# Kernel tuning notes

Hardware: AMD Instinct MI355X
Metric: run time of the kernel (lower is better)

Reference implementation:

```python
import jax, jax.numpy as jnp
import numpy as np

B, E, F = 16384, 128, 6
ITEM_V, CATE_V, HIST = 91718, 11, 50
I_IDX, J_IDX = np.triu_indices(F, k=1)  # 15 field pairs, loop order (0,1),(0,2),...
EPS = 1e-5


def _xavier(key, shape):
    fan_in, fan_out = shape[0], shape[-1]
    std = (2.0 / (fan_in + fan_out)) ** 0.5
    return std * jax.random.normal(key, shape, dtype=jnp.float32)


def setup_inputs() -> dict:
    key = jax.random.key(0)
    ks = jax.random.split(key, 20)
    inp = {
        'item_id': jax.random.randint(ks[0], (B,), 0, ITEM_V),
        'item_emb_d128': jax.random.normal(ks[1], (B, 128), dtype=jnp.float32),
        'likes_level': jax.random.randint(ks[2], (B,), 0, CATE_V),
        'views_level': jax.random.randint(ks[3], (B,), 0, CATE_V),
        'item_seq': jax.random.randint(ks[4], (B, HIST), 0, ITEM_V),
        # learned parameters
        'item_emb': 0.05 * jax.random.normal(ks[5], (ITEM_V, E), dtype=jnp.float32),
        'cate_emb': 0.05 * jax.random.normal(ks[6], (CATE_V, E), dtype=jnp.float32),
        'mm_W': _xavier(ks[7], (128, E)), 'mm_b': jnp.zeros((E,), jnp.float32),
        'ln_g': jnp.ones((E,), jnp.float32), 'ln_b': jnp.zeros((E,), jnp.float32),
        'se_W1': _xavier(ks[8], (F, F // 2)), 'se_b1': jnp.zeros((F // 2,), jnp.float32),
        'se_W2': _xavier(ks[9], (F // 2, F)), 'se_b2': jnp.zeros((F,), jnp.float32),
        'bi_W': _xavier(ks[10], (E, E)),
        'mlp_W1': _xavier(ks[11], (21 * E, 512)), 'mlp_b1': jnp.zeros((512,), jnp.float32),
        'bn1_g': jnp.ones((512,), jnp.float32), 'bn1_b': jnp.zeros((512,), jnp.float32),
        'bn1_rm': jnp.zeros((512,), jnp.float32), 'bn1_rv': jnp.ones((512,), jnp.float32),
        'mlp_W2': _xavier(ks[12], (512, 256)), 'mlp_b2': jnp.zeros((256,), jnp.float32),
        'bn2_g': jnp.ones((256,), jnp.float32), 'bn2_b': jnp.zeros((256,), jnp.float32),
        'bn2_rm': jnp.zeros((256,), jnp.float32), 'bn2_rv': jnp.ones((256,), jnp.float32),
        'mlp_W3': _xavier(ks[13], (256, 1)), 'mlp_b3': jnp.zeros((1,), jnp.float32),
    }
    return inp


def _forward(item_id, item_emb_d128, likes_level, views_level, item_seq,
             item_emb, cate_emb, mm_W, mm_b, ln_g, ln_b,
             se_W1, se_b1, se_W2, se_b2, bi_W,
             mlp_W1, mlp_b1, bn1_g, bn1_b, bn1_rm, bn1_rv,
             mlp_W2, mlp_b2, bn2_g, bn2_b, bn2_rm, bn2_rv,
             mlp_W3, mlp_b3):
    b = item_id.shape[0]
    tab = item_emb.at[0].set(0.0)  # padding_idx=0
    like_feat = cate_emb[likes_level]
    view_feat = cate_emb[views_level]
    item_feat = tab[item_id]
    # mm_proj: Linear -> LayerNorm -> ReLU
    mm = item_emb_d128 @ mm_W + mm_b
    mu = mm.mean(-1, keepdims=True)
    var = jnp.var(mm, axis=-1, keepdims=True)
    mm = jax.nn.relu((mm - mu) / jnp.sqrt(var + EPS) * ln_g + ln_b)
    # masked mean pooling over history
    seq_emb = tab[item_seq]                               # (B, HIST, E)
    valid = (item_seq != 0).astype(seq_emb.dtype)
    seq_sum = (seq_emb * valid[..., None]).sum(1)
    cnt = jnp.clip(valid.sum(1, keepdims=True), 1.0)
    hist_feat = seq_sum / cnt
    user_feat = jnp.zeros((b, E), seq_emb.dtype)
    x = jnp.stack([user_feat, like_feat, view_feat, item_feat, mm, hist_feat], axis=1)  # (B,6,E)
    # SENet
    z = x.mean(-1)
    w = jax.nn.sigmoid(jax.nn.relu(z @ se_W1 + se_b1) @ se_W2 + se_b2)
    xs = x * w[:, :, None]
    # bilinear 'all'
    xw = jnp.einsum('bfe,ed->bfd', xs, bi_W)
    p = xs[:, I_IDX, :] * xw[:, J_IDX, :]                 # (B,15,E)
    c = jnp.concatenate([xs.reshape(b, -1), p.reshape(b, -1)], axis=1)  # (B, 2688)
    # MLP head (eval mode: BN uses running stats, dropout off)
    h = c @ mlp_W1 + mlp_b1
    h = jax.nn.relu((h - bn1_rm) / jnp.sqrt(bn1_rv + EPS) * bn1_g + bn1_b)
    h = h @ mlp_W2 + mlp_b2
    h = jax.nn.relu((h - bn2_rm) / jnp.sqrt(bn2_rv + EPS) * bn2_g + bn2_b)
    logits = h @ mlp_W3 + mlp_b3
    return jax.nn.sigmoid(logits)[:, 0]


def reference(item_id, item_emb_d128, likes_level, views_level, item_seq,
              item_emb, cate_emb, mm_W, mm_b, ln_g, ln_b,
              se_W1, se_b1, se_W2, se_b2, bi_W,
              mlp_W1, mlp_b1, bn1_g, bn1_b, bn1_rm, bn1_rv,
              mlp_W2, mlp_b2, bn2_g, bn2_b, bn2_rm, bn2_rv,
              mlp_W3, mlp_b3):
    return _forward(item_id, item_emb_d128, likes_level, views_level, item_seq,
                    item_emb, cate_emb, mm_W, mm_b, ln_g, ln_b,
                    se_W1, se_b1, se_W2, se_b2, bi_W,
                    mlp_W1, mlp_b1, bn1_g, bn1_b, bn1_rm, bn1_rv,
                    mlp_W2, mlp_b2, bn2_g, bn2_b, bn2_rm, bn2_rv,
                    mlp_W3, mlp_b3)
```

## Files before the change

### kernel.cpp

```cpp
#include <hip/hip_runtime.h>
#include <hip/hip_bf16.h>

typedef __hip_bfloat16 bfloat;
typedef __bf16 bf16x8 __attribute__((ext_vector_type(8)));
typedef float f32x4 __attribute__((ext_vector_type(4)));

#define B_SZ   16384
#define E_DIM  128
#define HIST_L 50


#define IPACK 0x3221110000ULL
#define JPACK 0x3323213210ULL

__device__ __forceinline__ void gl_lds16(const void* g, void* l) {
    __builtin_amdgcn_global_load_lds(
        (const __attribute__((address_space(1))) unsigned int*)g,
        (__attribute__((address_space(3))) unsigned int*)l, 16, 0, 0);
}

__device__ __forceinline__ bf16x8 mul_bf16x8(bf16x8 a, bf16x8 b) {
    union { bf16x8 v; __hip_bfloat162 h[4]; } ua, ub, ur;
    ua.v = a; ub.v = b;
    #pragma unroll
    for (int i = 0; i < 4; ++i) ur.h[i] = __hmul2(ua.h[i], ub.h[i]);
    return ur.v;
}

__global__ __launch_bounds__(256) void feat_kernel(
    const int* __restrict__ item_id,
    const int* __restrict__ likes, const int* __restrict__ views,
    const int* __restrict__ seq,
    const float* __restrict__ item_emb, const float* __restrict__ cate_emb,
    const float* __restrict__ mm,
    const float* __restrict__ ln_g, const float* __restrict__ ln_b,
    const float* __restrict__ se_W1, const float* __restrict__ se_b1,
    const float* __restrict__ se_W2, const float* __restrict__ se_b2,
    bfloat* __restrict__ xs)
{
    const int tid = threadIdx.x;
    const int r   = tid >> 7;
    const int e   = tid & 127;
    const int b   = blockIdx.x * 2 + r;
    const int w   = tid >> 6;

    __shared__ float redh[2][4][128];
    __shared__ int   seq_s[2][64];
    __shared__ float lnred[4], lnred2[4];
    __shared__ float zred[5][4];
    __shared__ float wsh[2][6];
    __shared__ int   cnt_s[2];

    if (e < 64) seq_s[r][e] = (e < HIST_L) ? seq[(size_t)b * HIST_L + e] : 0;
    __syncthreads();

    const int iid = item_id[b];
    const float like_v = cate_emb[likes[b] * 128 + e];
    const float view_v = cate_emb[views[b] * 128 + e];
    const float item_raw = item_emb[(size_t)iid * 128 + e];
    const float item_v = iid ? item_raw : 0.f;
    const float acc = mm[(size_t)b * 128 + e];

    const int q   = e >> 5;
    const int l32 = e & 31;
    float4 hs = make_float4(0.f, 0.f, 0.f, 0.f);
    #pragma unroll
    for (int g = 0; g < 13; ++g) {
        int s = seq_s[r][g * 4 + q];
        const float4 v = *(const float4*)&item_emb[(size_t)s * 128 + l32 * 4];
        float m = (s != 0) ? 1.f : 0.f;
        hs.x = fmaf(v.x, m, hs.x);
        hs.y = fmaf(v.y, m, hs.y);
        hs.z = fmaf(v.z, m, hs.z);
        hs.w = fmaf(v.w, m, hs.w);
    }

    {
        float v = acc;
        #pragma unroll
        for (int off = 32; off > 0; off >>= 1) v += __shfl_down(v, off, 64);
        if ((tid & 63) == 0) lnred[w] = v;
    }
    __syncthreads();
    const float mu = (lnred[2 * r] + lnred[2 * r + 1]) * (1.f / 128.f);
    const float d  = acc - mu;
    {
        float v = d * d;
        #pragma unroll
        for (int off = 32; off > 0; off >>= 1) v += __shfl_down(v, off, 64);
        if ((tid & 63) == 0) lnred2[w] = v;
    }
    redh[r][q][l32 * 4 + 0] = hs.x;
    redh[r][q][l32 * 4 + 1] = hs.y;
    redh[r][q][l32 * 4 + 2] = hs.z;
    redh[r][q][l32 * 4 + 3] = hs.w;
    if ((w & 1) == 0 && e < 64) {
        bool valid = (e < HIST_L) && (seq_s[r][e] != 0);
        unsigned long long m = __ballot(valid);
        if (e == 0) cnt_s[r] = (int)__popcll(m);
    }
    __syncthreads();
    const float var = (lnred2[2 * r] + lnred2[2 * r + 1]) * (1.f / 128.f);
    float xmm = d * rsqrtf(var + 1e-5f) * ln_g[e] + ln_b[e];
    xmm = fmaxf(xmm, 0.f);

    const int cnt = cnt_s[r] > 0 ? cnt_s[r] : 1;
    const float hist_v = (redh[r][0][e] + redh[r][1][e] +
                          redh[r][2][e] + redh[r][3][e]) / (float)cnt;

    {
        float s1 = like_v, s2 = view_v, s3 = item_v, s4 = xmm, s5 = hist_v;
        #pragma unroll
        for (int off = 32; off > 0; off >>= 1) {
            s1 += __shfl_down(s1, off, 64);
            s2 += __shfl_down(s2, off, 64);
            s3 += __shfl_down(s3, off, 64);
            s4 += __shfl_down(s4, off, 64);
            s5 += __shfl_down(s5, off, 64);
        }
        if ((tid & 63) == 0) {
            zred[0][w] = s1; zred[1][w] = s2; zred[2][w] = s3;
            zred[3][w] = s4; zred[4][w] = s5;
        }
    }
    __syncthreads();

    if (e == 0) {
        float z[6];
        z[0] = 0.f;
        #pragma unroll
        for (int f = 1; f < 6; ++f)
            z[f] = (zred[f - 1][2 * r] + zred[f - 1][2 * r + 1]) * (1.f / 128.f);
        float a[3];
        #pragma unroll
        for (int j = 0; j < 3; ++j) {
            float s = se_b1[j];
            #pragma unroll
            for (int f = 0; f < 6; ++f) s += z[f] * se_W1[f * 3 + j];
            a[j] = fmaxf(s, 0.f);
        }
        #pragma unroll
        for (int f = 0; f < 6; ++f) {
            float s = se_b2[f];
            #pragma unroll
            for (int j = 0; j < 3; ++j) s += a[j] * se_W2[j * 6 + f];
            wsh[r][f] = 1.f / (1.f + expf(-s));
        }
    }
    __syncthreads();

    bfloat* xrow = xs + (size_t)b * 640;
    xrow[0 * 128 + e] = __float2bfloat16(like_v * wsh[r][1]);
    xrow[1 * 128 + e] = __float2bfloat16(view_v * wsh[r][2]);
    xrow[2 * 128 + e] = __float2bfloat16(item_v * wsh[r][3]);
    xrow[3 * 128 + e] = __float2bfloat16(xmm    * wsh[r][4]);
    xrow[4 * 128 + e] = __float2bfloat16(hist_v * wsh[r][5]);
}

__global__ __launch_bounds__(256) void transpose_f32_bf16(
    const float* __restrict__ in, bfloat* __restrict__ out, int K, int N)
{
    int idx = blockIdx.x * 256 + threadIdx.x;
    if (idx < K * N) {
        int k = idx / N, n = idx % N;
        out[(size_t)n * K + k] = __float2bfloat16(in[idx]);
    }
}

__global__ __launch_bounds__(256) void transpose_W1c(
    const float* __restrict__ W1, bfloat* __restrict__ W1t)
{
    int idx = blockIdx.x * 256 + threadIdx.x;
    if (idx < 512 * 1920) {
        int n = idx / 1920, kk = idx % 1920;
        int orig = kk + (kk < 640 ? 128 : 768);
        W1t[idx] = __float2bfloat16(W1[(size_t)orig * 512 + n]);
    }
}

__global__ __launch_bounds__(256) void bn_pre(
    const float* __restrict__ lb1, const float* __restrict__ g1,
    const float* __restrict__ bb1, const float* __restrict__ rm1,
    const float* __restrict__ rv1,
    const float* __restrict__ lb2, const float* __restrict__ g2,
    const float* __restrict__ bb2, const float* __restrict__ rm2,
    const float* __restrict__ rv2,
    const float* __restrict__ mm_b,
    float* __restrict__ S1, float* __restrict__ T1,
    float* __restrict__ S2, float* __restrict__ T2,
    float* __restrict__ Tmm)
{
    int j = blockIdx.x * 256 + threadIdx.x;
    if (j < 512) {
        float s = g1[j] * rsqrtf(rv1[j] + 1e-5f);
        S1[j] = s;
        T1[j] = (lb1[j] - rm1[j]) * s + bb1[j];
    } else if (j < 768) {
        int k = j - 512;
        float s = g2[k] * rsqrtf(rv2[k] + 1e-5f);
        S2[k] = s;
        T2[k] = (lb2[k] - rm2[k]) * s + bb2[k];
    } else if (j < 896) {
        Tmm[j - 768] = mm_b[j - 768];
    }
}

template<int MODE, int EPI, int MT, int NT, int F32OUT>
__global__ __launch_bounds__(256) void gemm_bt(
    const void* __restrict__ A, const bfloat* __restrict__ A2,
    const bfloat* __restrict__ Bt, void* __restrict__ C,
    int M, int N, int K,
    const float* __restrict__ S, const float* __restrict__ T)
{
    __shared__ __align__(16) short As[2][MT * 32];
    __shared__ __align__(16) short Bs[2][NT * 32];

    const int tid  = threadIdx.x;
    const int bm   = blockIdx.x * MT;
    const int bn   = blockIdx.y * NT;
    const int wave = tid >> 6;
    const int lane = tid & 63;
    const int wm   = (wave >> 1) * (MT / 2);
    const int wn   = (wave & 1) * (NT / 2);
    const int AF   = MT / 32;
    const int BF   = NT / 32;

    const short* Ag  = (const short*)A;
    const short* A2g = (const short*)A2;
    const short* Bg  = (const short*)Bt;

    f32x4 acc[MT / 32][NT / 32];
    #pragma unroll
    for (int i = 0; i < AF; ++i)
        #pragma unroll
        for (int j = 0; j < BF; ++j)
            acc[i][j] = (f32x4){0.f, 0.f, 0.f, 0.f};

    const int srow = tid >> 2;
    const int skc  = (tid & 3) * 8;

    for (int kt = 0; kt < K; kt += 64) {
        __syncthreads();
        #pragma unroll
        for (int h = 0; h < 2; ++h) {
            const int kk = kt + h * 32;
            #pragma unroll
            for (int r = 0; r < MT / 64; ++r) {
                int row = srow + r * 64;
                short* dst = &As[h][row * 32 + skc];
                if (MODE == 1) {
                    long rb = (long)(bm + row);
                    if (kk < 640) {
                        gl_lds16(&Ag[rb * 640 + kk + skc], dst);
                    } else {
                        int pp  = (kk - 640) >> 7;
                        int isl = (int)((IPACK >> (4 * pp)) & 15);
                        int jsl = (int)((JPACK >> (4 * pp)) & 15);
                        int e0  = ((kk - 640) & 127) + skc;
                        bf16x8 a = *(const bf16x8*)&Ag [rb * 640 + isl * 128 + e0];
                        bf16x8 b = *(const bf16x8*)&A2g[rb * 512 + jsl * 128 + e0];
                        *(bf16x8*)dst = mul_bf16x8(a, b);
                    }
                } else if (MODE == 2) {
                    int gr = bm + row;
                    gl_lds16(&Ag[((long)(gr >> 2)) * 640 +
                                 ((gr & 3) + 1) * 128 + kk + skc], dst);
                } else if (MODE == 3) {
                    const float* Af = (const float*)A;
                    long aoff = (long)(bm + row) * K + kk + skc;
                    float4 f0 = *(const float4*)&Af[aoff];
                    float4 f1 = *(const float4*)&Af[aoff + 4];
                    union { bf16x8 v; unsigned short s[8]; } u;
                    u.s[0] = __bfloat16_as_ushort(__float2bfloat16(f0.x));
                    u.s[1] = __bfloat16_as_ushort(__float2bfloat16(f0.y));
                    u.s[2] = __bfloat16_as_ushort(__float2bfloat16(f0.z));
                    u.s[3] = __bfloat16_as_ushort(__float2bfloat16(f0.w));
                    u.s[4] = __bfloat16_as_ushort(__float2bfloat16(f1.x));
                    u.s[5] = __bfloat16_as_ushort(__float2bfloat16(f1.y));
                    u.s[6] = __bfloat16_as_ushort(__float2bfloat16(f1.z));
                    u.s[7] = __bfloat16_as_ushort(__float2bfloat16(f1.w));
                    *(bf16x8*)dst = u.v;
                } else {
                    gl_lds16(&Ag[(long)(bm + row) * K + kk + skc], dst);
                }
            }
            #pragma unroll
            for (int r = 0; r < NT / 64; ++r) {
                int row = srow + r * 64;
                gl_lds16(&Bg[(long)(bn + row) * K + kk + skc],
                         &Bs[h][row * 32 + skc]);
            }
        }
        __syncthreads();

        const int koff  = (lane >> 4) * 8;
        const int rbase = lane & 15;
        #pragma unroll
        for (int h = 0; h < 2; ++h) {
            bf16x8 af[MT / 32], bfr[NT / 32];
            #pragma unroll
            for (int mt = 0; mt < AF; ++mt)
                af[mt] = *(const bf16x8*)
                    &As[h][(wm + mt * 16 + rbase) * 32 + koff];
            #pragma unroll
            for (int nt = 0; nt < BF; ++nt)
                bfr[nt] = *(const bf16x8*)
                    &Bs[h][(wn + nt * 16 + rbase) * 32 + koff];
            #pragma unroll
            for (int mt = 0; mt < AF; ++mt)
                #pragma unroll
                for (int nt = 0; nt < BF; ++nt)
                    acc[mt][nt] = __builtin_amdgcn_mfma_f32_16x16x32_bf16(
                        af[mt], bfr[nt], acc[mt][nt], 0, 0, 0);
        }
    }

    const int col0 = lane & 15;
    const int row0 = (lane >> 4) * 4;
    #pragma unroll
    for (int nt = 0; nt < BF; ++nt) {
        int col = bn + wn + nt * 16 + col0;
        float s = 1.f, t = 0.f;
        if (EPI) { s = (EPI == 1) ? S[col] : 1.f; t = T[col]; }
        #pragma unroll
        for (int mt = 0; mt < AF; ++mt) {
            #pragma unroll
            for (int i = 0; i < 4; ++i) {
                int row = bm + wm + mt * 16 + row0 + i;
                float v = acc[mt][nt][i];
                if (EPI == 1) v = fmaxf(v * s + t, 0.f);
                if (EPI == 2) v = v + t;
                if (F32OUT) ((float*)C)[(size_t)row * N + col] = v;
                else ((bfloat*)C)[(size_t)row * N + col] = __float2bfloat16(v);
            }
        }
    }
}

__global__ __launch_bounds__(256) void head_kernel(
    const bfloat* __restrict__ h2, const float* __restrict__ W3,
    const float* __restrict__ b3, float* __restrict__ out)
{
    int lane = threadIdx.x & 63;
    int row  = blockIdx.x * 4 + (threadIdx.x >> 6);
    float acc = 0.f;
    #pragma unroll
    for (int i = 0; i < 4; ++i)
        acc += __bfloat162float(h2[(size_t)row * 256 + i * 64 + lane]) *
               W3[i * 64 + lane];
    #pragma unroll
    for (int off = 32; off > 0; off >>= 1) acc += __shfl_down(acc, off, 64);
    if (lane == 0) {
        float l = acc + b3[0];
        out[row] = 1.f / (1.f + expf(-l));
    }
}

extern "C" void kernel_launch(void* const* d_in, const int* in_sizes, int n_in,
                              void* d_out, int out_size, void* d_ws, size_t ws_size,
                              hipStream_t stream) {
    const int*   item_id = (const int*)  d_in[0];
    const float* d128    = (const float*)d_in[1];
    const int*   likes   = (const int*)  d_in[2];
    const int*   views   = (const int*)  d_in[3];
    const int*   seq     = (const int*)  d_in[4];
    const float* item_emb= (const float*)d_in[5];
    const float* cate_emb= (const float*)d_in[6];
    const float* mm_W    = (const float*)d_in[7];
    const float* mm_b    = (const float*)d_in[8];
    const float* ln_g    = (const float*)d_in[9];
    const float* ln_b    = (const float*)d_in[10];
    const float* se_W1   = (const float*)d_in[11];
    const float* se_b1   = (const float*)d_in[12];
    const float* se_W2   = (const float*)d_in[13];
    const float* se_b2   = (const float*)d_in[14];
    const float* bi_W    = (const float*)d_in[15];
    const float* W1      = (const float*)d_in[16];
    const float* b1      = (const float*)d_in[17];
    const float* bn1_g   = (const float*)d_in[18];
    const float* bn1_b   = (const float*)d_in[19];
    const float* bn1_rm  = (const float*)d_in[20];
    const float* bn1_rv  = (const float*)d_in[21];
    const float* W2      = (const float*)d_in[22];
    const float* b2      = (const float*)d_in[23];
    const float* bn2_g   = (const float*)d_in[24];
    const float* bn2_b   = (const float*)d_in[25];
    const float* bn2_rm  = (const float*)d_in[26];
    const float* bn2_rv  = (const float*)d_in[27];
    const float* W3      = (const float*)d_in[28];
    const float* b3      = (const float*)d_in[29];

    const size_t fixed = 2300416;
    int CH = 1024;
    if      (fixed + (size_t)16384 * 3328 <= ws_size) CH = 16384;
    else if (fixed + (size_t)8192  * 3328 <= ws_size) CH = 8192;
    else if (fixed + (size_t)4096  * 3328 <= ws_size) CH = 4096;
    else if (fixed + (size_t)2048  * 3328 <= ws_size) CH = 2048;

    char* ws = (char*)d_ws;
    bfloat* W1t = (bfloat*)(ws);
    bfloat* W2t = (bfloat*)(ws + 1966080);
    bfloat* bWt = (bfloat*)(ws + 2228224);
    bfloat* mmWt= (bfloat*)(ws + 2260992);
    float*  S1  = (float*) (ws + 2293760);
    float*  T1  = (float*) (ws + 2295808);
    float*  S2  = (float*) (ws + 2297856);
    float*  T2  = (float*) (ws + 2298880);
    float*  Tmm = (float*) (ws + 2299904);
    bfloat* xs  = (bfloat*)(ws + fixed);
    bfloat* xw  = (bfloat*)(ws + fixed + (size_t)CH * 1280);
    bfloat* h1  = (bfloat*)(ws + fixed + (size_t)CH * 2304);
    bfloat* h2  = xw;
    float*  mm  = (float*)h1;

    transpose_W1c<<<(512 * 1920 + 255) / 256, 256, 0, stream>>>(W1, W1t);
    transpose_f32_bf16<<<(512 * 256 + 255) / 256, 256, 0, stream>>>(W2, W2t, 512, 256);
    transpose_f32_bf16<<<(128 * 128 + 255) / 256, 256, 0, stream>>>(bi_W, bWt, 128, 128);
    transpose_f32_bf16<<<(128 * 128 + 255) / 256, 256, 0, stream>>>(mm_W, mmWt, 128, 128);
    bn_pre<<<4, 256, 0, stream>>>(b1, bn1_g, bn1_b, bn1_rm, bn1_rv,
                                  b2, bn2_g, bn2_b, bn2_rm, bn2_rv,
                                  mm_b, S1, T1, S2, T2, Tmm);

    for (int off = 0; off < B_SZ; off += CH) {
        dim3 gmm(CH / 128, 128 / 64);
        gemm_bt<3, 2, 128, 64, 1><<<gmm, 256, 0, stream>>>(
            d128 + (size_t)off * 128, nullptr, mmWt, mm,
            CH, 128, 128, nullptr, Tmm);

        feat_kernel<<<CH / 2, 256, 0, stream>>>(
            item_id + off, likes + off, views + off,
            seq + (size_t)off * HIST_L, item_emb, cate_emb, mm,
            ln_g, ln_b, se_W1, se_b1, se_W2, se_b2, xs);

        dim3 gxw(CH * 4 / 128, 128 / 64);
        gemm_bt<2, 0, 128, 64, 0><<<gxw, 256, 0, stream>>>(
            xs, nullptr, bWt, xw, CH * 4, 128, 128, nullptr, nullptr);

        dim3 g1(CH / 128, 512 / 64);
        gemm_bt<1, 1, 128, 64, 0><<<g1, 256, 0, stream>>>(
            xs, xw, W1t, h1, CH, 512, 1920, S1, T1);

        dim3 g2(CH / 128, 256 / 64);
        gemm_bt<0, 1, 128, 64, 0><<<g2, 256, 0, stream>>>(
            h1, nullptr, W2t, h2, CH, 256, 512, S2, T2);

        head_kernel<<<CH / 4, 256, 0, stream>>>(h2, W3, b3, (float*)d_out + off);
    }
}
```

Measured before the change: 314.7 us.

## Double-buffer GEMM tiles with XOR-swizzled LDS layout

Restructures the bf16 MFMA GEMM so the next 64-wide K tile is staged into a second LDS buffer while the current one is consumed, with one barrier per iteration in place of two. The LDS tile layout becomes 64-column rows with an XOR swizzle on 16-byte chunks, applied both when staging from global memory and when reading fragments, to cut bank conflicts. The goal is to hide global load latency and reduce LDS conflicts. In exchange it doubles shared memory per block, which may lower occupancy, and adds index arithmetic.

After: 315.2 us. Within noise of the previous version (+0.2%).

```diff
diff --git a/kernel.cpp b/kernel.cpp
--- a/kernel.cpp
+++ b/kernel.cpp
@@ -212,8 +212,8 @@
     int M, int N, int K,
     const float* __restrict__ S, const float* __restrict__ T)
 {
-    __shared__ __align__(16) short As[2][MT * 32];
-    __shared__ __align__(16) short Bs[2][NT * 32];
+    __shared__ __align__(16) short As[2][MT * 64];
+    __shared__ __align__(16) short Bs[2][NT * 64];
 
     const int tid  = threadIdx.x;
     const int bm   = blockIdx.x * MT;
@@ -222,96 +222,122 @@
     const int lane = tid & 63;
     const int wm   = (wave >> 1) * (MT / 2);
     const int wn   = (wave & 1) * (NT / 2);
-    const int AF   = MT / 32;
-    const int BF   = NT / 32;
+    constexpr int AF = MT / 32;
+    constexpr int BF = NT / 32;
 
     const short* Ag  = (const short*)A;
     const short* A2g = (const short*)A2;
     const short* Bg  = (const short*)Bt;
 
-    f32x4 acc[MT / 32][NT / 32];
+    f32x4 acc[AF][BF];
     #pragma unroll
     for (int i = 0; i < AF; ++i)
         #pragma unroll
         for (int j = 0; j < BF; ++j)
             acc[i][j] = (f32x4){0.f, 0.f, 0.f, 0.f};
 
-    const int srow = tid >> 2;
-    const int skc  = (tid & 3) * 8;
-
-    for (int kt = 0; kt < K; kt += 64) {
-        __syncthreads();
+    const int srow = tid >> 3;
+    const int sck  = tid & 7;
+
+    auto stage = [&](int buf, int kt) {
+        #pragma unroll
+        for (int rr = 0; rr < NT / 32; ++rr) {
+            int row = srow + rr * 32;
+            int g   = sck ^ (row & 7);
+            gl_lds16(&Bg[(long)(bn + row) * K + kt + g * 8],
+                     &Bs[buf][row * 64 + sck * 8]);
+        }
+        if (MODE == 1 && kt >= 640) {
+            #pragma unroll
+            for (int rr = 0; rr < MT / 32; ++rr) {
+                int row = srow + rr * 32;
+                int g   = sck ^ (row & 7);
+                int kg  = kt - 640 + g * 8;
+                int pp  = kg >> 7;
+                int isl = (int)((IPACK >> (4 * pp)) & 15);
+                int jsl = (int)((JPACK >> (4 * pp)) & 15);
+                int e0  = kg & 127;
+                long rb = (long)(bm + row);
+                bf16x8 a = *(const bf16x8*)&Ag [rb * 640 + isl * 128 + e0];
+                bf16x8 b = *(const bf16x8*)&A2g[rb * 512 + jsl * 128 + e0];
+                *(bf16x8*)&As[buf][row * 64 + sck * 8] = mul_bf16x8(a, b);
+            }
+        } else if (MODE == 3) {
+            const float* Af = (const float*)A;
+            #pragma unroll
+            for (int rr = 0; rr < MT / 32; ++rr) {
+                int row = srow + rr * 32;
+                int g   = sck ^ (row & 7);
+                long aoff = (long)(bm + row) * K + kt + g * 8;
+                float4 f0 = *(const float4*)&Af[aoff];
+                float4 f1 = *(const float4*)&Af[aoff + 4];
+                union { bf16x8 v; unsigned short s[8]; } u;
+                u.s[0] = __bfloat16_as_ushort(__float2bfloat16(f0.x));
+                u.s[1] = __bfloat16_as_ushort(__float2bfloat16(f0.y));
+                u.s[2] = __bfloat16_as_ushort(__float2bfloat16(f0.z));
+                u.s[3] = __bfloat16_as_ushort(__float2bfloat16(f0.w));
+                u.s[4] = __bfloat16_as_ushort(__float2bfloat16(f1.x));
+                u.s[5] = __bfloat16_as_ushort(__float2bfloat16(f1.y));
+                u.s[6] = __bfloat16_as_ushort(__float2bfloat16(f1.z));
+                u.s[7] = __bfloat16_as_ushort(__float2bfloat16(f1.w));
+                *(bf16x8*)&As[buf][row * 64 + sck * 8] = u.v;
+            }
+        } else {
+            #pragma unroll
+            for (int rr = 0; rr < MT / 32; ++rr) {
+                int row = srow + rr * 32;
+                int g   = sck ^ (row & 7);
+                const short* src;
+                if (MODE == 2) {
+                    int gr = bm + row;
+                    src = &Ag[((long)(gr >> 2)) * 640 +
+                              ((gr & 3) + 1) * 128 + kt + g * 8];
+                } else if (MODE == 1) {
+                    src = &Ag[(long)(bm + row) * 640 + kt + g * 8];
+                } else {
+                    src = &Ag[(long)(bm + row) * K + kt + g * 8];
+                }
+                gl_lds16(src, &As[buf][row * 64 + sck * 8]);
+            }
+        }
+    };
+
+    const int rbase = lane & 15;
+    const int cswz  = rbase & 7;
+
+    const int nk = K >> 6;
+    stage(0, 0);
+    asm volatile("s_waitcnt vmcnt(0) lgkmcnt(0)" ::: "memory");
+    __builtin_amdgcn_s_barrier();
+
+    for (int i = 0; i < nk; ++i) {
+        const int cur = i & 1;
+        if (i + 1 < nk) stage(cur ^ 1, (i + 1) << 6);
+
         #pragma unroll
         for (int h = 0; h < 2; ++h) {
-            const int kk = kt + h * 32;
-            #pragma unroll
-            for (int r = 0; r < MT / 64; ++r) {
-                int row = srow + r * 64;
-                short* dst = &As[h][row * 32 + skc];
-                if (MODE == 1) {
-                    long rb = (long)(bm + row);
-                    if (kk < 640) {
-                        gl_lds16(&Ag[rb * 640 + kk + skc], dst);
-                    } else {
-                        int pp  = (kk - 640) >> 7;
-                        int isl = (int)((IPACK >> (4 * pp)) & 15);
-                        int jsl = (int)((JPACK >> (4 * pp)) & 15);
-                        int e0  = ((kk - 640) & 127) + skc;
-                        bf16x8 a = *(const bf16x8*)&Ag [rb * 640 + isl * 128 + e0];
-                        bf16x8 b = *(const bf16x8*)&A2g[rb * 512 + jsl * 128 + e0];
-                        *(bf16x8*)dst = mul_bf16x8(a, b);
-                    }
-                } else if (MODE == 2) {
-                    int gr = bm + row;
-                    gl_lds16(&Ag[((long)(gr >> 2)) * 640 +
-                                 ((gr & 3) + 1) * 128 + kk + skc], dst);
-                } else if (MODE == 3) {
-                    const float* Af = (const float*)A;
-                    long aoff = (long)(bm + row) * K + kk + skc;
-                    float4 f0 = *(const float4*)&Af[aoff];
-                    float4 f1 = *(const float4*)&Af[aoff + 4];
-                    union { bf16x8 v; unsigned short s[8]; } u;
-                    u.s[0] = __bfloat16_as_ushort(__float2bfloat16(f0.x));
-                    u.s[1] = __bfloat16_as_ushort(__float2bfloat16(f0.y));
-                    u.s[2] = __bfloat16_as_ushort(__float2bfloat16(f0.z));
-                    u.s[3] = __bfloat16_as_ushort(__float2bfloat16(f0.w));
-                    u.s[4] = __bfloat16_as_ushort(__float2bfloat16(f1.x));
-                    u.s[5] = __bfloat16_as_ushort(__float2bfloat16(f1.y));
-                    u.s[6] = __bfloat16_as_ushort(__float2bfloat16(f1.z));
-                    u.s[7] = __bfloat16_as_ushort(__float2bfloat16(f1.w));
-                    *(bf16x8*)dst = u.v;
-                } else {
-                    gl_lds16(&Ag[(long)(bm + row) * K + kk + skc], dst);
-                }
-            }
-            #pragma unroll
-            for (int r = 0; r < NT / 64; ++r) {
-                int row = srow + r * 64;
-                gl_lds16(&Bg[(long)(bn + row) * K + kk + skc],
-                         &Bs[h][row * 32 + skc]);
-            }
-        }
-        __syncthreads();
-
-        const int koff  = (lane >> 4) * 8;
-        const int rbase = lane & 15;
-        #pragma unroll
-        for (int h = 0; h < 2; ++h) {
-            bf16x8 af[MT / 32], bfr[NT / 32];
+            const int cg = h * 4 + (lane >> 4);
+            const int ca = (cg ^ cswz) << 3;
+            bf16x8 af[AF], bfr[BF];
             #pragma unroll
             for (int mt = 0; mt < AF; ++mt)
                 af[mt] = *(const bf16x8*)
-                    &As[h][(wm + mt * 16 + rbase) * 32 + koff];
+                    &As[cur][(wm + mt * 16 + rbase) * 64 + ca];
             #pragma unroll
             for (int nt = 0; nt < BF; ++nt)
                 bfr[nt] = *(const bf16x8*)
-                    &Bs[h][(wn + nt * 16 + rbase) * 32 + koff];
+                    &Bs[cur][(wn + nt * 16 + rbase) * 64 + ca];
             #pragma unroll
             for (int mt = 0; mt < AF; ++mt)
                 #pragma unroll
                 for (int nt = 0; nt < BF; ++nt)
                     acc[mt][nt] = __builtin_amdgcn_mfma_f32_16x16x32_bf16(
                         af[mt], bfr[nt], acc[mt][nt], 0, 0, 0);
+        }
+
+        if (i + 1 < nk) {
+            asm volatile("s_waitcnt vmcnt(0) lgkmcnt(0)" ::: "memory");
+            __builtin_amdgcn_s_barrier();
         }
     }
 
```
